# Performance work log

Hardware: AMD Instinct MI355X
Metric: run time of the kernel (lower is better)

Reference implementation:

```python
import jax, jax.numpy as jnp
import numpy as np

B, H, S, D = 2, 8, 4096, 64


def setup_inputs() -> dict:
    key = jax.random.key(0)
    kq, kk, kv = jax.random.split(key, 3)
    q = jax.random.normal(kq, (B, H, S, D), dtype=jnp.float32)
    k = jax.random.normal(kk, (B, H, S, D), dtype=jnp.float32)
    v = jax.random.normal(kv, (B, H, S, D), dtype=jnp.float32)
    return {"q": q, "k": k, "v": v}


def reference(q, k, v):
    # attn = q @ k^T  (unnormalized, no softmax), out = attn @ v
    attn = jnp.einsum("bhqd,bhkd->bhqk", q, k)
    out = jnp.einsum("bhqk,bhkd->bhqd", attn, v)
    return out
```

## Files before the change

### kernel.cpp

```cpp
#include <hip/hip_runtime.h>
#include <hip/hip_bf16.h>


#define SD 262144
#define SDIM 4096
#define DDIM 64
#define NH 16
#define NCHUNK 64
#define CHUNK 64

typedef short bf16x8 __attribute__((ext_vector_type(8)));
typedef float f32x16 __attribute__((ext_vector_type(16)));

__device__ __forceinline__ unsigned short f2bf(float f) {
    unsigned int u = __float_as_uint(f);
    u += 0x7fffu + ((u >> 16) & 1u);
    return (unsigned short)(u >> 16);
}

__device__ __forceinline__ float bf2f(unsigned short h) {
    return __uint_as_float((unsigned int)h << 16);
}

union frag_cast { bf16x8 v; __hip_bfloat162 h[4]; };

__global__ __launch_bounds__(256) void ktv_mfma(const float* __restrict__ Kp,
                                                const float* __restrict__ Vp,
                                                unsigned short* __restrict__ part) {
    __shared__ float ldsK[CHUNK * DDIM];
    __shared__ float ldsV[CHUNK * DDIM];

    const int g = blockIdx.x;
    const int h = g >> 6;
    const int c = g & 63;
    const size_t base = (size_t)h * SD + (size_t)c * CHUNK * DDIM;

    const int w = threadIdx.x >> 6;
    const int l = threadIdx.x & 63;
    const int l31 = l & 31;
    const int kg = (l >> 5) * 8;
    const int dh = (w >> 1) * 32;
    const int eh = (w & 1) * 32;

    const float* Ksrc = Kp + base;
    const float* Vsrc = Vp + base;
#pragma unroll
    for (int i = 0; i < 4; ++i) {
        const int seg = w * 4 + i;
        __builtin_amdgcn_global_load_lds(
            (const __attribute__((address_space(1))) void*)(Ksrc + seg * 256 + l * 4),
            (__attribute__((address_space(3))) void*)(ldsK + seg * 256),
            16, 0, 0);
        __builtin_amdgcn_global_load_lds(
            (const __attribute__((address_space(1))) void*)(Vsrc + seg * 256 + l * 4),
            (__attribute__((address_space(3))) void*)(ldsV + seg * 256),
            16, 0, 0);
    }
    __syncthreads();

    f32x16 acc = {};
#pragma unroll
    for (int s0 = 0; s0 < CHUNK; s0 += 16) {
        frag_cast ua, ub;
#pragma unroll
        for (int j = 0; j < 4; ++j) {
            const int r0 = (s0 + kg + 2 * j) * DDIM;
            const int r1 = (s0 + kg + 2 * j + 1) * DDIM;
            ua.h[j] = __float22bfloat162_rn(float2{ldsV[r0 + dh + l31],
                                                   ldsV[r1 + dh + l31]});
            ub.h[j] = __float22bfloat162_rn(float2{ldsK[r0 + eh + l31],
                                                   ldsK[r1 + eh + l31]});
        }
        acc = __builtin_amdgcn_mfma_f32_32x32x16_bf16(ua.v, ub.v, acc, 0, 0, 0);
    }

    unsigned short* pg = part + (size_t)g * 4096;
#pragma unroll
    for (int r = 0; r < 16; ++r) {
        const int d = (r & 3) + 8 * (r >> 2) + 4 * (l >> 5) + dh;
        pg[(size_t)d * DDIM + eh + l31] = f2bf(acc[r]);
    }
}

__global__ __launch_bounds__(256) void reduce_mt(const unsigned short* __restrict__ part,
                                                 unsigned short* __restrict__ mt) {
    const int b = blockIdx.x;
    const int h = b >> 4;
    const int d = (b & 15) * 4 + (threadIdx.x >> 6);
    const int e = threadIdx.x & 63;
    const unsigned short* ph = part + (size_t)h * NCHUNK * 4096 + d * 64 + e;
    float s = 0.f;
#pragma unroll
    for (int c = 0; c < NCHUNK; ++c) s += bf2f(ph[(size_t)c * 4096]);
    mt[(size_t)h * 4096 + d * 64 + e] = f2bf(s);
}

__global__ __launch_bounds__(256) void qm_gemm(const float* __restrict__ Qp,
                                               const unsigned short* __restrict__ mt,
                                               float* __restrict__ out) {
    const int bx = blockIdx.x;
    const int h = bx >> 5;
    const int qt = bx & 31;
    const int w = threadIdx.x >> 6;
    const int l = threadIdx.x & 63;
    const int l31 = l & 31;
    const int kg = (l >> 5) * 8;

    const float* Qh = Qp + (size_t)h * SD + (size_t)(qt * 128 + w * 32) * DDIM;
    const unsigned short* Mh = mt + (size_t)h * 4096;

    bf16x8 a[4];
#pragma unroll
    for (int kk = 0; kk < 4; ++kk) {
        const float4* q4 = (const float4*)(Qh + (size_t)l31 * DDIM + kk * 16 + kg);
        const float4 q0 = q4[0], q1 = q4[1];
        frag_cast u;
        u.h[0] = __float22bfloat162_rn(float2{q0.x, q0.y});
        u.h[1] = __float22bfloat162_rn(float2{q0.z, q0.w});
        u.h[2] = __float22bfloat162_rn(float2{q1.x, q1.y});
        u.h[3] = __float22bfloat162_rn(float2{q1.z, q1.w});
        a[kk] = u.v;
    }

    f32x16 acc0 = {};
    f32x16 acc1 = {};
#pragma unroll
    for (int kk = 0; kk < 4; ++kk) {
        const bf16x8 b0 = *(const bf16x8*)(Mh + (size_t)l31 * 64 + kk * 16 + kg);
        const bf16x8 b1 = *(const bf16x8*)(Mh + (size_t)(l31 + 32) * 64 + kk * 16 + kg);
        acc0 = __builtin_amdgcn_mfma_f32_32x32x16_bf16(a[kk], b0, acc0, 0, 0, 0);
        acc1 = __builtin_amdgcn_mfma_f32_32x32x16_bf16(a[kk], b1, acc1, 0, 0, 0);
    }

    float* Oh = out + (size_t)h * SD + (size_t)(qt * 128 + w * 32) * DDIM;
#pragma unroll
    for (int r = 0; r < 16; ++r) {
        const int row = (r & 3) + 8 * (r >> 2) + 4 * (l >> 5);
        Oh[(size_t)row * DDIM + l31] = acc0[r];
        Oh[(size_t)row * DDIM + 32 + l31] = acc1[r];
    }
}

extern "C" void kernel_launch(void* const* d_in, const int* in_sizes, int n_in,
                              void* d_out, int out_size, void* d_ws, size_t ws_size,
                              hipStream_t stream) {
    const float* q = (const float*)d_in[0];
    const float* k = (const float*)d_in[1];
    const float* v = (const float*)d_in[2];
    float* out = (float*)d_out;

    unsigned short* part = (unsigned short*)d_ws;
    unsigned short* mt =
        (unsigned short*)((char*)d_ws + (size_t)NH * NCHUNK * 4096 * 2);

    ktv_mfma<<<NH * NCHUNK, 256, 0, stream>>>(k, v, part);
    reduce_mt<<<256, 256, 0, stream>>>(part, mt);
    qm_gemm<<<NH * 32, 256, 0, stream>>>(q, mt, out);
}
```

Measured before the change: 24.55 us.

## Replace partial-sum reduction kernel with fp32 atomic accumulation of K^T V

The chunked K^T V kernel now atomically adds its fp32 tile into a per-head 64x64 accumulator instead of writing bf16 partials that a separate reduction kernel sums. A small zeroing kernel is added up front. The Q·M GEMM reads the fp32 matrix, converts it to bf16 in registers, and uses twice as many blocks, each computing one 32-column half. This removes the partial-buffer traffic and one kernel's work, but brings heavy atomic contention (64 chunks per head hitting the same addresses) and makes the summation order nondeterministic.

```diff
diff --git a/kernel.cpp b/kernel.cpp
--- a/kernel.cpp
+++ b/kernel.cpp
@@ -12,21 +12,15 @@
 typedef short bf16x8 __attribute__((ext_vector_type(8)));
 typedef float f32x16 __attribute__((ext_vector_type(16)));
 
-__device__ __forceinline__ unsigned short f2bf(float f) {
-    unsigned int u = __float_as_uint(f);
-    u += 0x7fffu + ((u >> 16) & 1u);
-    return (unsigned short)(u >> 16);
+union frag_cast { bf16x8 v; __hip_bfloat162 h[4]; };
+
+__global__ __launch_bounds__(256) void zero_m(float* __restrict__ m) {
+    m[blockIdx.x * 256 + threadIdx.x] = 0.f;
 }
-
-__device__ __forceinline__ float bf2f(unsigned short h) {
-    return __uint_as_float((unsigned int)h << 16);
-}
-
-union frag_cast { bf16x8 v; __hip_bfloat162 h[4]; };
 
 __global__ __launch_bounds__(256) void ktv_mfma(const float* __restrict__ Kp,
                                                 const float* __restrict__ Vp,
-                                                unsigned short* __restrict__ part) {
+                                                float* __restrict__ m32) {
     __shared__ float ldsK[CHUNK * DDIM];
     __shared__ float ldsV[CHUNK * DDIM];
 
@@ -74,70 +68,55 @@
         acc = __builtin_amdgcn_mfma_f32_32x32x16_bf16(ua.v, ub.v, acc, 0, 0, 0);
     }
 
-    unsigned short* pg = part + (size_t)g * 4096;
+    float* mh = m32 + (size_t)h * 4096;
 #pragma unroll
     for (int r = 0; r < 16; ++r) {
         const int d = (r & 3) + 8 * (r >> 2) + 4 * (l >> 5) + dh;
-        pg[(size_t)d * DDIM + eh + l31] = f2bf(acc[r]);
+        atomicAdd(&mh[d * DDIM + eh + l31], acc[r]);
     }
 }
 
-__global__ __launch_bounds__(256) void reduce_mt(const unsigned short* __restrict__ part,
-                                                 unsigned short* __restrict__ mt) {
-    const int b = blockIdx.x;
-    const int h = b >> 4;
-    const int d = (b & 15) * 4 + (threadIdx.x >> 6);
-    const int e = threadIdx.x & 63;
-    const unsigned short* ph = part + (size_t)h * NCHUNK * 4096 + d * 64 + e;
-    float s = 0.f;
-#pragma unroll
-    for (int c = 0; c < NCHUNK; ++c) s += bf2f(ph[(size_t)c * 4096]);
-    mt[(size_t)h * 4096 + d * 64 + e] = f2bf(s);
-}
-
 __global__ __launch_bounds__(256) void qm_gemm(const float* __restrict__ Qp,
-                                               const unsigned short* __restrict__ mt,
+                                               const float* __restrict__ m32,
                                                float* __restrict__ out) {
     const int bx = blockIdx.x;
-    const int h = bx >> 5;
-    const int qt = bx & 31;
+    const int h = bx >> 6;
+    const int qt = bx & 63;
     const int w = threadIdx.x >> 6;
     const int l = threadIdx.x & 63;
     const int l31 = l & 31;
     const int kg = (l >> 5) * 8;
+    const int ch = (w & 1) * 32;
+    const int rowbase = qt * 64 + (w >> 1) * 32;
 
-    const float* Qh = Qp + (size_t)h * SD + (size_t)(qt * 128 + w * 32) * DDIM;
-    const unsigned short* Mh = mt + (size_t)h * 4096;
+    const float* Qh = Qp + (size_t)h * SD + (size_t)rowbase * DDIM;
+    const float* Mh = m32 + (size_t)h * 4096;
 
-    bf16x8 a[4];
+    f32x16 acc = {};
 #pragma unroll
     for (int kk = 0; kk < 4; ++kk) {
         const float4* q4 = (const float4*)(Qh + (size_t)l31 * DDIM + kk * 16 + kg);
         const float4 q0 = q4[0], q1 = q4[1];
-        frag_cast u;
-        u.h[0] = __float22bfloat162_rn(float2{q0.x, q0.y});
-        u.h[1] = __float22bfloat162_rn(float2{q0.z, q0.w});
-        u.h[2] = __float22bfloat162_rn(float2{q1.x, q1.y});
-        u.h[3] = __float22bfloat162_rn(float2{q1.z, q1.w});
-        a[kk] = u.v;
+        frag_cast ua;
+        ua.h[0] = __float22bfloat162_rn(float2{q0.x, q0.y});
+        ua.h[1] = __float22bfloat162_rn(float2{q0.z, q0.w});
+        ua.h[2] = __float22bfloat162_rn(float2{q1.x, q1.y});
+        ua.h[3] = __float22bfloat162_rn(float2{q1.z, q1.w});
+        const float4* m4 = (const float4*)(Mh + (size_t)(ch + l31) * DDIM + kk * 16 + kg);
+        const float4 m0 = m4[0], m1 = m4[1];
+        frag_cast ub;
+        ub.h[0] = __float22bfloat162_rn(float2{m0.x, m0.y});
+        ub.h[1] = __float22bfloat162_rn(float2{m0.z, m0.w});
+        ub.h[2] = __float22bfloat162_rn(float2{m1.x, m1.y});
+        ub.h[3] = __float22bfloat162_rn(float2{m1.z, m1.w});
+        acc = __builtin_amdgcn_mfma_f32_32x32x16_bf16(ua.v, ub.v, acc, 0, 0, 0);
     }
 
-    f32x16 acc0 = {};
-    f32x16 acc1 = {};
-#pragma unroll
-    for (int kk = 0; kk < 4; ++kk) {
-        const bf16x8 b0 = *(const bf16x8*)(Mh + (size_t)l31 * 64 + kk * 16 + kg);
-        const bf16x8 b1 = *(const bf16x8*)(Mh + (size_t)(l31 + 32) * 64 + kk * 16 + kg);
-        acc0 = __builtin_amdgcn_mfma_f32_32x32x16_bf16(a[kk], b0, acc0, 0, 0, 0);
-        acc1 = __builtin_amdgcn_mfma_f32_32x32x16_bf16(a[kk], b1, acc1, 0, 0, 0);
-    }
-
-    float* Oh = out + (size_t)h * SD + (size_t)(qt * 128 + w * 32) * DDIM;
+    float* Oh = out + (size_t)h * SD + (size_t)rowbase * DDIM;
 #pragma unroll
     for (int r = 0; r < 16; ++r) {
         const int row = (r & 3) + 8 * (r >> 2) + 4 * (l >> 5);
-        Oh[(size_t)row * DDIM + l31] = acc0[r];
-        Oh[(size_t)row * DDIM + 32 + l31] = acc1[r];
+        Oh[(size_t)row * DDIM + ch + l31] = acc[r];
     }
 }
 
@@ -149,11 +128,9 @@
     const float* v = (const float*)d_in[2];
     float* out = (float*)d_out;
 
-    unsigned short* part = (unsigned short*)d_ws;
-    unsigned short* mt =
-        (unsigned short*)((char*)d_ws + (size_t)NH * NCHUNK * 4096 * 2);
+    float* m32 = (float*)d_ws;
 
-    ktv_mfma<<<NH * NCHUNK, 256, 0, stream>>>(k, v, part);
-    reduce_mt<<<256, 256, 0, stream>>>(part, mt);
-    qm_gemm<<<NH * 32, 256, 0, stream>>>(q, mt, out);
+    zero_m<<<NH * 4096 / 256, 256, 0, stream>>>(m32);
+    ktv_mfma<<<NH * NCHUNK, 256, 0, stream>>>(k, v, m32);
+    qm_gemm<<<NH * 64, 256, 0, stream>>>(q, m32, out);
 }
```

Result: slower. 38.47 us (+56.7%).
